# Performance work log

Measured on AMD Instinct MI355X. Metric: run time of the kernel, lower is better.

Reference implementation:

```python
import jax, jax.numpy as jnp
import numpy as np

H, D, K = 8, 64, 9           # new num heads, head size, conv kernel size
A = H * D                    # all_head_size = 512
HID = 2 * A                  # input hidden size = 1024
STD = 0.02


def setup_inputs() -> dict:
    key = jax.random.key(0)
    ks = jax.random.split(key, 16)
    B, S = 4, 2048
    f = jnp.float32
    inp = {
        'hidden_states': jax.random.normal(ks[0], (B, S, HID), f),
        'Wq': jax.random.normal(ks[1], (A, A), f) * STD,
        'bq': jnp.zeros((A,), f),
        'Wk': jax.random.normal(ks[2], (A, A), f) * STD,
        'bk': jnp.zeros((A,), f),
        'Wv': jax.random.normal(ks[3], (A, A), f) * STD,
        'bv': jnp.zeros((A,), f),
        'dw_w': jax.random.normal(ks[4], (A, 1, K), f) * STD,   # depthwise conv (groups=A)
        'pw_w': jax.random.normal(ks[5], (A, A, 1), f) * STD,   # pointwise 1x1 conv
        'sep_b': jnp.zeros((A, 1), f),                          # SeparableConv1D bias
        'Wck': jax.random.normal(ks[6], (H * K, A), f) * STD,   # conv_kernel_layer
        'bck': jnp.zeros((H * K,), f),
        'Wco': jax.random.normal(ks[7], (A, A), f) * STD,       # conv_out_layer
        'bco': jnp.zeros((A,), f),
    }
    return inp


def reference(hidden_states, Wq, bq, Wk, bk, Wv, bv, dw_w, pw_w, sep_b, Wck, bck, Wco, bco):
    B, S, _ = hidden_states.shape
    hs_attn = hidden_states[:, :, :A]
    hs_conv = hidden_states[:, :, A:]

    q = hs_attn @ Wq.T + bq
    k = hs_attn @ Wk.T + bk
    v = hs_attn @ Wv.T + bv

    # SeparableConv1D on (B, A, S): depthwise then pointwise, plus bias
    x = hs_conv.transpose(0, 2, 1)
    x = jax.lax.conv_general_dilated(
        x, dw_w, window_strides=(1,), padding=[(K // 2, K // 2)],
        feature_group_count=A, dimension_numbers=('NCH', 'OIH', 'NCH'))
    x = jnp.einsum('bcs,oc->bos', x, pw_w[:, :, 0]) + sep_b
    mixed_key_conv = x.transpose(0, 2, 1)            # (B,S,A)

    # per-token softmax conv kernel
    conv_attn = mixed_key_conv * hs_conv
    ckl = (conv_attn @ Wck.T + bck).reshape(B, S, H, K)
    ckl = jax.nn.softmax(ckl, axis=-1)               # softmax over kernel taps

    # dynamic-span lightweight convolution (unfold -> batched matmul)
    col = hs_conv @ Wco.T + bco                      # (B,S,A)
    pad = jnp.pad(col, ((0, 0), (K // 2, K // 2), (0, 0)))
    windows = jnp.stack([pad[:, i:i + S] for i in range(K)], axis=-1)  # (B,S,A,K)
    windows = windows.reshape(B, S, H, D, K)
    conv_out = jnp.einsum('bshdk,bshk->bshd', windows, ckl)            # (B,S,H,D)

    # standard self-attention
    qh = q.reshape(B, S, H, D).transpose(0, 2, 1, 3)
    kh = k.reshape(B, S, H, D).transpose(0, 2, 1, 3)
    vh = v.reshape(B, S, H, D).transpose(0, 2, 1, 3)
    scale = jnp.asarray(1.0 / np.sqrt(D), q.dtype)
    scores = jnp.einsum('bhqd,bhkd->bhqk', qh, kh) * scale
    probs = jax.nn.softmax(scores, axis=-1)
    ctx = jnp.einsum('bhqk,bhkd->bqhd', probs, vh)   # (B,S,H,D)

    out = jnp.concatenate([ctx, conv_out], axis=2)   # (B,S,2H,D)
    return out.reshape(B, S, HID)
```

## Files before the change

kernel.cpp:

```cpp
#include <hip/hip_runtime.h>
#include <hip/hip_bf16.h>

#define NH   8
#define HD   64
#define KW   9
#define AD   512
#define HIDD 1024
#define BB   4
#define SS   2048
#define MTOK (BB*SS)
#define WSZ  262144

typedef __attribute__((ext_vector_type(8))) short short8;
typedef __attribute__((ext_vector_type(4))) float floatx4;
typedef __attribute__((ext_vector_type(16))) float floatx16;

__device__ __forceinline__ short f2bf(float f) {
    unsigned u = __float_as_uint(f);
    u = (u + 0x7FFFu + ((u >> 16) & 1u)) >> 16;
    return (short)u;
}
__device__ __forceinline__ float bf2f(short s) {
    return __uint_as_float(((unsigned)(unsigned short)s) << 16);
}
__device__ __forceinline__ float exp2_raw(float x) {
    return __builtin_amdgcn_exp2f(x);
}
__device__ __forceinline__ unsigned pkbf2(float a, float b) {
    unsigned d;
    asm("v_cvt_pk_bf16_f32 %0, %1, %2" : "=v"(d) : "v"(a), "v"(b));
    return d;
}
__device__ __forceinline__ void gl2lds16(const short* g, short* l) {
    __builtin_amdgcn_global_load_lds(
        (const __attribute__((address_space(1))) void*)g,
        (__attribute__((address_space(3))) void*)l, 16, 0, 0);
}

__global__ __launch_bounds__(256) void prep_kernel(
    const float* __restrict__ hs,
    const float* __restrict__ pw, const float* __restrict__ Wco,
    const float* __restrict__ Wq, const float* __restrict__ Wk,
    const float* __restrict__ Wv, const float* __restrict__ Wck,
    const float* __restrict__ dw,
    short* __restrict__ hsb, short* __restrict__ wb, short* __restrict__ x1)
{
    __shared__ float wl[KW * AD];
    const int bid = blockIdx.x, tid = threadIdx.x;

    if (bid < 4096) {
        int idx = bid * 256 + tid;
        const float* s = hs + (long)idx * 8;
        float4 a = *(const float4*)s, c = *(const float4*)(s + 4);
        short8 o;
        o[0]=f2bf(a.x); o[1]=f2bf(a.y); o[2]=f2bf(a.z); o[3]=f2bf(a.w);
        o[4]=f2bf(c.x); o[5]=f2bf(c.y); o[6]=f2bf(c.z); o[7]=f2bf(c.w);
        *(short8*)(hsb + (long)idx * 8) = o;
    } else if (bid < 4768) {
        int idx = (bid - 4096) * 256 + tid;
        int e0 = idx * 8;
        short8 o;
        if (e0 < 5 * WSZ) {
            int w = e0 >> 18, off = e0 & (WSZ - 1);
            const float* src = (w == 0) ? pw : (w == 1) ? Wco : (w == 2) ? Wq
                             : (w == 3) ? Wk : Wv;
            float4 a = *(const float4*)(src + off), c = *(const float4*)(src + off + 4);
            o[0]=f2bf(a.x); o[1]=f2bf(a.y); o[2]=f2bf(a.z); o[3]=f2bf(a.w);
            o[4]=f2bf(c.x); o[5]=f2bf(c.y); o[6]=f2bf(c.z); o[7]=f2bf(c.w);
        } else {
            int off = e0 - 5 * WSZ;
            int row = off >> 9, col = off & 511;
            if (row < NH * KW) {
                const float* src = Wck + row * AD + col;
                float4 a = *(const float4*)src, c = *(const float4*)(src + 4);
                o[0]=f2bf(a.x); o[1]=f2bf(a.y); o[2]=f2bf(a.z); o[3]=f2bf(a.w);
                o[4]=f2bf(c.x); o[5]=f2bf(c.y); o[6]=f2bf(c.z); o[7]=f2bf(c.w);
            } else {
                for (int i = 0; i < 8; ++i) o[i] = 0;
            }
        }
        *(short8*)(wb + e0) = o;
    } else {
        for (int t = tid; t < KW * AD; t += 256) {
            int c = t / KW, k = t - c * KW;
            wl[k * AD + c] = dw[t];
        }
        __syncthreads();
        int idx = (bid - 4768) * 256 + tid;
        int c8  = (idx & 63) * 8;
        int tok = idx >> 6;
        int s   = tok & (SS - 1);
        int b   = tok >> 11;
        const float* base = hs + (long)(b * SS) * HIDD + AD + c8;
        float acc[8];
#pragma unroll
        for (int i = 0; i < 8; ++i) acc[i] = 0.f;
#pragma unroll
        for (int kk = 0; kk < KW; ++kk) {
            int ss2 = s + kk - KW / 2;
            if (ss2 >= 0 && ss2 < SS) {
                const float* hp = base + (long)ss2 * HIDD;
                float4 h0 = *(const float4*)hp;
                float4 h1 = *(const float4*)(hp + 4);
                float4 w0 = *(const float4*)(wl + kk * AD + c8);
                float4 w1 = *(const float4*)(wl + kk * AD + c8 + 4);
                acc[0] += w0.x * h0.x; acc[1] += w0.y * h0.y;
                acc[2] += w0.z * h0.z; acc[3] += w0.w * h0.w;
                acc[4] += w1.x * h1.x; acc[5] += w1.y * h1.y;
                acc[6] += w1.z * h1.z; acc[7] += w1.w * h1.w;
            }
        }
        short8 o;
#pragma unroll
        for (int i = 0; i < 8; ++i) o[i] = f2bf(acc[i]);
        *(short8*)(x1 + (long)tok * AD + c8) = o;
    }
}

template<int FM, int FN, int MODE>
__device__ __forceinline__ void gemm_body(
    int bx, int by, short* As, short* Bs,
    const short* __restrict__ X, int ldx, int xoff,
    const short* __restrict__ W,
    const float* __restrict__ b0p, const float* __restrict__ b1p,
    const float* __restrict__ b2p,
    const short* __restrict__ mulp, int mul_ld, int mul_off,
    void* __restrict__ Cout, short* __restrict__ vtout,
    int ldc, int N, int Kd, float oscale)
{
    constexpr int TM = 32 * FM, TN = 32 * FN;
    const int tid  = threadIdx.x;
    const int wv   = tid >> 6, lane = tid & 63;
    const int ln   = lane & 15, quad = lane >> 4;
    const int wm   = wv >> 1, wn = wv & 1;
    const int m0 = bx * TM, n0 = by * TN;

    floatx4 acc[FM][FN];
#pragma unroll
    for (int i = 0; i < FM; ++i)
#pragma unroll
        for (int j = 0; j < FN; ++j) acc[i][j] = (floatx4){0.f, 0.f, 0.f, 0.f};

    const short* xbase = X + (long)m0 * ldx + xoff;
    const short* wbase = W + (long)n0 * Kd;

    for (int k0 = 0; k0 < Kd; k0 += 64) {
#pragma unroll
        for (int g = tid; g < TM * 8; g += 256) {
            int m = g >> 3, p = g & 7, gk = p ^ (m & 7);
            gl2lds16(xbase + (long)m * ldx + k0 + gk * 8, &As[g * 8]);
        }
#pragma unroll
        for (int g = tid; g < TN * 8; g += 256) {
            int m = g >> 3, p = g & 7, gk = p ^ (m & 7);
            gl2lds16(wbase + (long)m * Kd + k0 + gk * 8, &Bs[g * 8]);
        }
        __syncthreads();
#pragma unroll
        for (int half = 0; half < 2; ++half) {
            short8 afr[FM], bfr[FN];
#pragma unroll
            for (int i = 0; i < FM; ++i) {
                int p = (half * 4 + quad) ^ (ln & 7);
                afr[i] = *(const short8*)&As[(wm * 16 * FM + i * 16 + ln) * 64 + p * 8];
            }
#pragma unroll
            for (int j = 0; j < FN; ++j) {
                int p = (half * 4 + quad) ^ (ln & 7);
                bfr[j] = *(const short8*)&Bs[(wn * 16 * FN + j * 16 + ln) * 64 + p * 8];
            }
#pragma unroll
            for (int i = 0; i < FM; ++i)
#pragma unroll
                for (int j = 0; j < FN; ++j)
                    acc[i][j] = __builtin_amdgcn_mfma_f32_16x16x32_bf16(
                        afr[i], bfr[j], acc[i][j], 0, 0, 0);
        }
        __syncthreads();
    }

#pragma unroll
    for (int j = 0; j < FN; ++j) {
        int n = n0 + wn * 16 * FN + j * 16 + ln;
        if constexpr (MODE == 3) {
            if (n >= 1024) {
                int hh = (n - 1024) >> 6, dd = (n - 1024) & 63;
                float bv = b2p[n - 1024];
                int mblk = m0 + wm * 16 * FM;
                int bidx = mblk >> 11, sblk = mblk & (SS - 1);
                short* dst = vtout + ((long)((bidx * NH + hh) * HD + dd)) * SS + sblk;
#pragma unroll
                for (int i = 0; i < FM; ++i) {
                    unsigned lo = pkbf2(acc[i][j][0] + bv, acc[i][j][1] + bv);
                    unsigned hi = pkbf2(acc[i][j][2] + bv, acc[i][j][3] + bv);
                    *(uint2*)(dst + i * 16 + quad * 4) = make_uint2(lo, hi);
                }
            } else {
                float bv = (n < 512) ? b0p[n] : b1p[n - 512];
                float sc = (n < 512) ? oscale : 1.f;
#pragma unroll
                for (int i = 0; i < FM; ++i) {
#pragma unroll
                    for (int r = 0; r < 4; ++r) {
                        int m = m0 + wm * 16 * FM + i * 16 + quad * 4 + r;
                        float val = (acc[i][j][r] + bv) * sc;
                        ((short*)Cout)[(long)m * ldc + n] = f2bf(val);
                    }
                }
            }
        } else if (n < N) {
            float bv = b0p[n], sc = oscale;
#pragma unroll
            for (int i = 0; i < FM; ++i) {
#pragma unroll
                for (int r = 0; r < 4; ++r) {
                    int m = m0 + wm * 16 * FM + i * 16 + quad * 4 + r;
                    float val = (acc[i][j][r] + bv) * sc;
                    if constexpr (MODE == 2)
                        val *= bf2f(mulp[(long)m * mul_ld + mul_off + n]);
                    if constexpr (MODE == 0)
                        ((float*)Cout)[(long)m * ldc + n] = val;
                    else
                        ((short*)Cout)[(long)m * ldc + n] = f2bf(val);
                }
            }
        }
    }
}

__global__ __launch_bounds__(256) void mega1_kernel(
    const short* __restrict__ hsb, const short* __restrict__ x1c,
    const short* __restrict__ Wqkv_b, const short* __restrict__ pw_b,
    const float* __restrict__ bq, const float* __restrict__ bk,
    const float* __restrict__ bv, const float* __restrict__ sepb,
    short* __restrict__ qkvb, short* __restrict__ vTb,
    short* __restrict__ cabO, float oscale)
{
    __shared__ __align__(16) short As[128 * 64];
    __shared__ __align__(16) short Bs[128 * 64];
    int bid = blockIdx.x;
    if (bid < 768) {
        gemm_body<4, 4, 3>(bid & 63, bid >> 6, As, Bs,
            hsb, HIDD, 0, Wqkv_b, bq, bk, bv, nullptr, 0, 0,
            qkvb, vTb, 1536, 1536, AD, oscale);
    } else {
        int id = bid - 768;
        gemm_body<4, 2, 2>(id & 63, id >> 6, As, Bs,
            x1c, AD, 0, pw_b, sepb, nullptr, nullptr, hsb, HIDD, AD,
            cabO, nullptr, AD, AD, AD, 1.f);
    }
}

__global__ __launch_bounds__(256) void mega2_kernel(
    const short* __restrict__ hsb, const short* __restrict__ cabO,
    const short* __restrict__ Wco_b, const short* __restrict__ Wck_b,
    const float* __restrict__ bco, const float* __restrict__ bck,
    short* __restrict__ x1c, float* __restrict__ ckl)
{
    __shared__ __align__(16) short As[128 * 64];
    __shared__ __align__(16) short Bs[128 * 64];
    int bid = blockIdx.x;
    if (bid < 512) {
        gemm_body<4, 2, 1>(bid & 63, bid >> 6, As, Bs,
            hsb, HIDD, AD, Wco_b, bco, nullptr, nullptr, nullptr, 0, 0,
            x1c, nullptr, AD, AD, AD, 1.f);
    } else {
        int id = bid - 512;
        gemm_body<2, 2, 0>(id & 127, id >> 7, As, Bs,
            cabO, AD, 0, Wck_b, bck, nullptr, nullptr, nullptr, 0, 0,
            ckl, nullptr, NH * KW, NH * KW, AD, 1.f);
    }
}

__global__ __launch_bounds__(256) void convout_kernel(
    const short* __restrict__ col, const float* __restrict__ ckl,
    float* __restrict__ out)
{
    int idx = blockIdx.x * 256 + threadIdx.x;
    int d4  = (idx & 127) * 4;
    int tok = idx >> 7;
    int s   = tok & (SS - 1);
    int b   = tok >> 11;
    int h   = d4 >> 6;
    const float* lg = ckl + (long)tok * (NH * KW) + h * KW;
    float wv[KW];
    float mx = -1e30f;
#pragma unroll
    for (int i = 0; i < KW; ++i) { wv[i] = lg[i]; mx = fmaxf(mx, wv[i]); }
    float sum = 0.f;
#pragma unroll
    for (int i = 0; i < KW; ++i) { wv[i] = __expf(wv[i] - mx); sum += wv[i]; }
    float inv = 1.f / sum;
    float a0 = 0.f, a1 = 0.f, a2 = 0.f, a3 = 0.f;
    const short* cbase = col + (long)(b * SS) * AD + d4;
#pragma unroll
    for (int kk = 0; kk < KW; ++kk) {
        int ss2 = s + kk - KW / 2;
        if (ss2 >= 0 && ss2 < SS) {
            uint2 cv = *(const uint2*)(cbase + (long)ss2 * AD);
            float w = wv[kk];
            a0 += w * bf2f((short)(cv.x & 0xFFFF));
            a1 += w * bf2f((short)(cv.x >> 16));
            a2 += w * bf2f((short)(cv.y & 0xFFFF));
            a3 += w * bf2f((short)(cv.y >> 16));
        }
    }
    *(float4*)&out[(long)tok * HIDD + AD + d4] =
        make_float4(a0 * inv, a1 * inv, a2 * inv, a3 * inv);
}

__global__ __launch_bounds__(256) void flash_mfma_kernel(
    const short* __restrict__ qkv, const short* __restrict__ vT,
    float* __restrict__ out)
{
    const int qt = blockIdx.x, h = blockIdx.y, b = blockIdx.z;
    const int tid  = threadIdx.x;
    const int w    = tid >> 6;
    const int lane = tid & 63;
    const int l5   = lane & 31;
    const int hh   = lane >> 5;

    __shared__ __align__(16) short Kb[3][4096];
    __shared__ __align__(16) short Vb[3][4096];
    __shared__ float ls[4][32];

    const int  q0 = qt * 128 + w * 32;
    const long rowbase = (long)b * SS;

    short8 qf[4];
    {
        const short* qrow = qkv + (rowbase + q0 + l5) * 1536 + h * HD;
#pragma unroll
        for (int i = 0; i < 4; ++i)
            qf[i] = *(const short8*)(qrow + i * 16 + hh * 8);
    }

    floatx16 acc0, acc1;
    floatx16 Z;
#pragma unroll
    for (int r = 0; r < 16; ++r) { acc0[r] = 0.f; acc1[r] = 0.f; Z[r] = 0.f; }
    float l_i = 0.f;

    const int m1 = tid >> 3,  gk1 = (tid & 7) ^ (m1 & 7);
    const int g2 = 256 + tid;
    const int m2 = g2 >> 3,   gk2 = (g2 & 7) ^ (m2 & 7);
    const short* kbase  = qkv + 512 + rowbase * 1536 + h * HD;
    const short* vtbase = vT + ((long)(b * NH + h) * HD) * SS;
    const short* sk0 = kbase  + (long)m1 * 1536 + gk1 * 8;
    const short* sk1 = kbase  + (long)m2 * 1536 + gk2 * 8;
    const short* sv0 = vtbase + (long)m1 * SS   + gk1 * 8;
    const short* sv1 = vtbase + (long)m2 * SS   + gk2 * 8;

    auto STAGE_K = [&](int slot, bool adv) {
        gl2lds16(sk0, &Kb[slot][tid * 8]);
        gl2lds16(sk1, &Kb[slot][g2 * 8]);
        if (adv) { sk0 += 64 * 1536; sk1 += 64 * 1536; }
    };
    auto STAGE_V = [&](int slot) {
        gl2lds16(sv0, &Vb[slot][tid * 8]);
        gl2lds16(sv1, &Vb[slot][g2 * 8]);
        sv0 += 64; sv1 += 64;
    };

    auto qkt = [&](const short* KB, floatx16& S0, floatx16& S1) {
        {
            int p = hh ^ (l5 & 7);
            short8 k0 = *(const short8*)&KB[l5 * 64 + p * 8];
            short8 k1 = *(const short8*)&KB[(32 + l5) * 64 + p * 8];
            S0 = __builtin_amdgcn_mfma_f32_32x32x16_bf16(k0, qf[0], Z, 0, 0, 0);
            S1 = __builtin_amdgcn_mfma_f32_32x32x16_bf16(k1, qf[0], Z, 0, 0, 0);
        }
#pragma unroll
        for (int i = 1; i < 4; ++i) {
            int p = (2 * i + hh) ^ (l5 & 7);
            short8 k0 = *(const short8*)&KB[l5 * 64 + p * 8];
            short8 k1 = *(const short8*)&KB[(32 + l5) * 64 + p * 8];
            S0 = __builtin_amdgcn_mfma_f32_32x32x16_bf16(k0, qf[i], S0, 0, 0, 0);
            S1 = __builtin_amdgcn_mfma_f32_32x32x16_bf16(k1, qf[i], S1, 0, 0, 0);
        }
    };

    auto smax = [&](const floatx16& S0, const floatx16& S1, short8* pf) {
        float pe0[16], pe1[16];
#pragma unroll
        for (int r = 0; r < 16; ++r) {
            pe0[r] = exp2_raw(S0[r]);
            pe1[r] = exp2_raw(S1[r]);
        }
        float s = 0.f;
#pragma unroll
        for (int r = 0; r < 16; ++r) s += pe0[r] + pe1[r];
        l_i += s;
#pragma unroll
        for (int t = 0; t < 2; ++t) {
            const float* pe = t ? pe1 : pe0;
#pragma unroll
            for (int u = 0; u < 2; ++u) {
                unsigned a0 = pkbf2(pe[8 * u + 0], pe[8 * u + 1]);
                unsigned a1 = pkbf2(pe[8 * u + 2], pe[8 * u + 3]);
                unsigned b0 = pkbf2(pe[8 * u + 4], pe[8 * u + 5]);
                unsigned b1 = pkbf2(pe[8 * u + 6], pe[8 * u + 7]);
                asm("v_permlane32_swap_b32 %0, %1" : "+v"(a0), "+v"(b0));
                asm("v_permlane32_swap_b32 %0, %1" : "+v"(a1), "+v"(b1));
                union { uint4 u4; short8 s8; } cv;
                cv.u4 = make_uint4(a0, a1, b0, b1);
                pf[t * 2 + u] = cv.s8;
            }
        }
    };

    auto pv = [&](const short* VB, const short8* pf) {
#pragma unroll
        for (int s = 0; s < 4; ++s) {
            int p = (2 * s + hh) ^ (l5 & 7);
            short8 v0 = *(const short8*)&VB[l5 * 64 + p * 8];
            short8 v1 = *(const short8*)&VB[(32 + l5) * 64 + p * 8];
            acc0 = __builtin_amdgcn_mfma_f32_32x32x16_bf16(pf[s], v0, acc0, 0, 0, 0);
            acc1 = __builtin_amdgcn_mfma_f32_32x32x16_bf16(pf[s], v1, acc1, 0, 0, 0);
        }
    };

    short8 pfA[4], pfB[4];

    STAGE_K(0, true);
    STAGE_K(1, true);
    STAGE_V(0);
    asm volatile("s_waitcnt vmcnt(0)" ::: "memory");
    __builtin_amdgcn_s_barrier();
    asm volatile("" ::: "memory");

    {
        STAGE_K(2, true);
        STAGE_V(1);
        floatx16 S0, S1;
        qkt(Kb[0], S0, S1);
        smax(S0, S1, pfA);
        asm volatile("s_waitcnt vmcnt(4)" ::: "memory");
        __builtin_amdgcn_s_barrier();
        asm volatile("" ::: "memory");
    }

#define PHASE(KS, VPS, KST, VST, KADV, PIN, POUT)                      \
    {                                                                  \
        STAGE_K(KST, KADV);                                            \
        STAGE_V(VST);                                                  \
        floatx16 S0, S1;                                               \
        __builtin_amdgcn_s_setprio(1);                                 \
        qkt(Kb[KS], S0, S1);                                           \
        pv(Vb[VPS], PIN);                                              \
        __builtin_amdgcn_s_setprio(0);                                 \
        smax(S0, S1, POUT);                                            \
        asm volatile("s_waitcnt vmcnt(4)" ::: "memory");               \
        __builtin_amdgcn_s_barrier();                                  \
        asm volatile("" ::: "memory");                                 \
    }

    for (int g = 0; g < 5; ++g) {
        bool notlast = (g < 4);
        PHASE(1, 0, 0, 2, true,    pfA, pfB);
        PHASE(2, 1, 1, 0, true,    pfB, pfA);
        PHASE(0, 2, 2, 1, true,    pfA, pfB);
        PHASE(1, 0, 0, 2, true,    pfB, pfA);
        PHASE(2, 1, 1, 0, notlast, pfA, pfB);
        PHASE(0, 2, 2, 1, notlast, pfB, pfA);
    }
#undef PHASE

    {
        floatx16 S0, S1;
        __builtin_amdgcn_s_setprio(1);
        qkt(Kb[1], S0, S1);
        pv(Vb[0], pfA);
        __builtin_amdgcn_s_setprio(0);
        smax(S0, S1, pfB);
        asm volatile("s_waitcnt vmcnt(0)" ::: "memory");
        __builtin_amdgcn_s_barrier();
        asm volatile("" ::: "memory");
    }
    pv(Vb[1], pfB);

    l_i += __shfl_xor(l_i, 32);
    ls[w][l5] = 1.f / l_i;
    float4 lv[4];
#pragma unroll
    for (int g = 0; g < 4; ++g)
        lv[g] = *(const float4*)&ls[w][8 * g + 4 * hh];

#pragma unroll
    for (int r = 0; r < 16; ++r) {
        int g = r >> 2, j = r & 3;
        int qr = j + 8 * g + 4 * hh;
        float iv = lv[g][j];
        float* orow = out + (rowbase + q0 + qr) * HIDD + h * HD;
        orow[l5]      = acc0[r] * iv;
        orow[32 + l5] = acc1[r] * iv;
    }
}

extern "C" void kernel_launch(void* const* d_in, const int* in_sizes, int n_in,
                              void* d_out, int out_size, void* d_ws, size_t ws_size,
                              hipStream_t stream)
{
    const float* hs   = (const float*)d_in[0];
    const float* Wq   = (const float*)d_in[1];
    const float* bq   = (const float*)d_in[2];
    const float* Wk   = (const float*)d_in[3];
    const float* bk   = (const float*)d_in[4];
    const float* Wv   = (const float*)d_in[5];
    const float* bv   = (const float*)d_in[6];
    const float* dw   = (const float*)d_in[7];
    const float* pw   = (const float*)d_in[8];
    const float* sepb = (const float*)d_in[9];
    const float* Wck  = (const float*)d_in[10];
    const float* bck  = (const float*)d_in[11];
    const float* Wco  = (const float*)d_in[12];
    const float* bco  = (const float*)d_in[13];
    float* out = (float*)d_out;

    short* hsb  = (short*)d_ws;
    short* x1c  = hsb + (long)MTOK * HIDD;
    short* qkvb = x1c + (long)MTOK * AD;
    short* vTb  = qkvb + (long)MTOK * 1536;
    float* ckl  = (float*)(vTb + (long)MTOK * AD);
    short* wb   = (short*)(ckl + (long)MTOK * (NH * KW));
    short* pw_b   = wb;
    short* Wco_b  = wb + 1L * WSZ;
    short* Wqkv_b = wb + 2L * WSZ;
    short* Wck_b  = wb + 5L * WSZ;
    short* cabO   = (short*)d_out;

    const float QSCALE = 0.18033688011112042f;

    prep_kernel<<<6816, 256, 0, stream>>>(
        hs, pw, Wco, Wq, Wk, Wv, Wck, dw, hsb, wb, x1c);
    mega1_kernel<<<1280, 256, 0, stream>>>(
        hsb, x1c, Wqkv_b, pw_b, bq, bk, bv, sepb, qkvb, vTb, cabO, QSCALE);
    mega2_kernel<<<768, 256, 0, stream>>>(
        hsb, cabO, Wco_b, Wck_b, bco, bck, x1c, ckl);
    convout_kernel<<<MTOK * AD / 1024, 256, 0, stream>>>(x1c, ckl, out);
    flash_mfma_kernel<<<dim3(SS / 128, NH, BB), 256, 0, stream>>>(qkvb, vTb, out);

    (void)in_sizes; (void)n_in; (void)out_size; (void)ws_size;
}
```

Measured before the change: 212.6 us.

## Fuse conv-out and flash attention into one 512-thread tail kernel

Merges the lightweight-conv output kernel and the flash attention kernel into a single launch. The first 256 blocks run attention and the remaining 2048 blocks run the conv-out. Each attention block now has 8 waves covering 256 queries, and each thread stages one K and one V chunk per tile instead of two, so the waitcnt thresholds drop to match. This removes a launch and lets the memory-bound conv work overlap with the MFMA-bound attention. In exchange there are fewer, larger attention blocks, which may cut occupancy and load balance.

```diff
diff --git a/kernel.cpp b/kernel.cpp
--- a/kernel.cpp
+++ b/kernel.cpp
@@ -272,59 +272,60 @@
     }
 }
 
-__global__ __launch_bounds__(256) void convout_kernel(
-    const short* __restrict__ col, const float* __restrict__ ckl,
+__global__ __launch_bounds__(512) void tail_kernel(
+    const short* __restrict__ qkv, const short* __restrict__ vT,
+    const short* __restrict__ colb, const float* __restrict__ cklp,
     float* __restrict__ out)
 {
-    int idx = blockIdx.x * 256 + threadIdx.x;
-    int d4  = (idx & 127) * 4;
-    int tok = idx >> 7;
-    int s   = tok & (SS - 1);
-    int b   = tok >> 11;
-    int h   = d4 >> 6;
-    const float* lg = ckl + (long)tok * (NH * KW) + h * KW;
-    float wv[KW];
-    float mx = -1e30f;
-#pragma unroll
-    for (int i = 0; i < KW; ++i) { wv[i] = lg[i]; mx = fmaxf(mx, wv[i]); }
-    float sum = 0.f;
-#pragma unroll
-    for (int i = 0; i < KW; ++i) { wv[i] = __expf(wv[i] - mx); sum += wv[i]; }
-    float inv = 1.f / sum;
-    float a0 = 0.f, a1 = 0.f, a2 = 0.f, a3 = 0.f;
-    const short* cbase = col + (long)(b * SS) * AD + d4;
-#pragma unroll
-    for (int kk = 0; kk < KW; ++kk) {
-        int ss2 = s + kk - KW / 2;
-        if (ss2 >= 0 && ss2 < SS) {
-            uint2 cv = *(const uint2*)(cbase + (long)ss2 * AD);
-            float w = wv[kk];
-            a0 += w * bf2f((short)(cv.x & 0xFFFF));
-            a1 += w * bf2f((short)(cv.x >> 16));
-            a2 += w * bf2f((short)(cv.y & 0xFFFF));
-            a3 += w * bf2f((short)(cv.y >> 16));
-        }
-    }
-    *(float4*)&out[(long)tok * HIDD + AD + d4] =
-        make_float4(a0 * inv, a1 * inv, a2 * inv, a3 * inv);
-}
-
-__global__ __launch_bounds__(256) void flash_mfma_kernel(
-    const short* __restrict__ qkv, const short* __restrict__ vT,
-    float* __restrict__ out)
-{
-    const int qt = blockIdx.x, h = blockIdx.y, b = blockIdx.z;
-    const int tid  = threadIdx.x;
+    __shared__ __align__(16) short Kb[3][4096];
+    __shared__ __align__(16) short Vb[3][4096];
+    __shared__ float ls[8][32];
+
+    const int bid = blockIdx.x;
+    const int tid = threadIdx.x;
+
+    if (bid >= 256) {
+        int idx = (bid - 256) * 512 + tid;
+        int d4  = (idx & 127) * 4;
+        int tok = idx >> 7;
+        int s   = tok & (SS - 1);
+        int b   = tok >> 11;
+        int h   = d4 >> 6;
+        const float* lg = cklp + (long)tok * (NH * KW) + h * KW;
+        float wv[KW];
+        float mx = -1e30f;
+#pragma unroll
+        for (int i = 0; i < KW; ++i) { wv[i] = lg[i]; mx = fmaxf(mx, wv[i]); }
+        float sum = 0.f;
+#pragma unroll
+        for (int i = 0; i < KW; ++i) { wv[i] = __expf(wv[i] - mx); sum += wv[i]; }
+        float inv = 1.f / sum;
+        float a0 = 0.f, a1 = 0.f, a2 = 0.f, a3 = 0.f;
+        const short* cbase = colb + (long)(b * SS) * AD + d4;
+#pragma unroll
+        for (int kk = 0; kk < KW; ++kk) {
+            int ss2 = s + kk - KW / 2;
+            if (ss2 >= 0 && ss2 < SS) {
+                uint2 cv = *(const uint2*)(cbase + (long)ss2 * AD);
+                float w = wv[kk];
+                a0 += w * bf2f((short)(cv.x & 0xFFFF));
+                a1 += w * bf2f((short)(cv.x >> 16));
+                a2 += w * bf2f((short)(cv.y & 0xFFFF));
+                a3 += w * bf2f((short)(cv.y >> 16));
+            }
+        }
+        *(float4*)&out[(long)tok * HIDD + AD + d4] =
+            make_float4(a0 * inv, a1 * inv, a2 * inv, a3 * inv);
+        return;
+    }
+
+    const int qt = bid & 7, h = (bid >> 3) & 7, b = bid >> 6;
     const int w    = tid >> 6;
     const int lane = tid & 63;
     const int l5   = lane & 31;
     const int hh   = lane >> 5;
 
-    __shared__ __align__(16) short Kb[3][4096];
-    __shared__ __align__(16) short Vb[3][4096];
-    __shared__ float ls[4][32];
-
-    const int  q0 = qt * 128 + w * 32;
+    const int  q0 = qt * 256 + w * 32;
     const long rowbase = (long)b * SS;
 
     short8 qf[4];
@@ -341,25 +342,19 @@
     for (int r = 0; r < 16; ++r) { acc0[r] = 0.f; acc1[r] = 0.f; Z[r] = 0.f; }
     float l_i = 0.f;
 
-    const int m1 = tid >> 3,  gk1 = (tid & 7) ^ (m1 & 7);
-    const int g2 = 256 + tid;
-    const int m2 = g2 >> 3,   gk2 = (g2 & 7) ^ (m2 & 7);
+    const int m1 = tid >> 3, gk1 = (tid & 7) ^ (m1 & 7);
     const short* kbase  = qkv + 512 + rowbase * 1536 + h * HD;
     const short* vtbase = vT + ((long)(b * NH + h) * HD) * SS;
     const short* sk0 = kbase  + (long)m1 * 1536 + gk1 * 8;
-    const short* sk1 = kbase  + (long)m2 * 1536 + gk2 * 8;
     const short* sv0 = vtbase + (long)m1 * SS   + gk1 * 8;
-    const short* sv1 = vtbase + (long)m2 * SS   + gk2 * 8;
 
     auto STAGE_K = [&](int slot, bool adv) {
         gl2lds16(sk0, &Kb[slot][tid * 8]);
-        gl2lds16(sk1, &Kb[slot][g2 * 8]);
-        if (adv) { sk0 += 64 * 1536; sk1 += 64 * 1536; }
+        if (adv) sk0 += 64 * 1536;
     };
     auto STAGE_V = [&](int slot) {
         gl2lds16(sv0, &Vb[slot][tid * 8]);
-        gl2lds16(sv1, &Vb[slot][g2 * 8]);
-        sv0 += 64; sv1 += 64;
+        sv0 += 64;
     };
 
     auto qkt = [&](const short* KB, floatx16& S0, floatx16& S1) {
@@ -435,7 +430,7 @@
         floatx16 S0, S1;
         qkt(Kb[0], S0, S1);
         smax(S0, S1, pfA);
-        asm volatile("s_waitcnt vmcnt(4)" ::: "memory");
+        asm volatile("s_waitcnt vmcnt(2)" ::: "memory");
         __builtin_amdgcn_s_barrier();
         asm volatile("" ::: "memory");
     }
@@ -450,7 +445,7 @@
         pv(Vb[VPS], PIN);                                              \
         __builtin_amdgcn_s_setprio(0);                                 \
         smax(S0, S1, POUT);                                            \
-        asm volatile("s_waitcnt vmcnt(4)" ::: "memory");               \
+        asm volatile("s_waitcnt vmcnt(2)" ::: "memory");               \
         __builtin_amdgcn_s_barrier();                                  \
         asm volatile("" ::: "memory");                                 \
     }
@@ -537,8 +532,7 @@
         hsb, x1c, Wqkv_b, pw_b, bq, bk, bv, sepb, qkvb, vTb, cabO, QSCALE);
     mega2_kernel<<<768, 256, 0, stream>>>(
         hsb, cabO, Wco_b, Wck_b, bco, bck, x1c, ckl);
-    convout_kernel<<<MTOK * AD / 1024, 256, 0, stream>>>(x1c, ckl, out);
-    flash_mfma_kernel<<<dim3(SS / 128, NH, BB), 256, 0, stream>>>(qkvb, vTb, out);
+    tail_kernel<<<2304, 512, 0, stream>>>(qkvb, vTb, x1c, ckl, out);
 
     (void)in_sizes; (void)n_in; (void)out_size; (void)ws_size;
 }
```

Result: slower. 223.2 us (+5.0%).

## Co-schedule flash attention with Wco/Wck GEMMs in one launch

Applied to the files above, without the earlier changes.

Merges the flash-attention kernel and the Wco and Wck projection GEMMs into a single kernel, mega3. Blocks 0–511 run attention and the rest run the GEMMs, so the GEMM work can fill the tail of the attention kernel and one launch is removed. The intermediate cabO buffer is moved into the conv half of the output rows (row stride 2048 shorts), so concurrent attention writes to the attn half cannot clobber it. The pointwise GEMM in mega1 switches to 4x4 tiles, which halves its block count. The risks are load imbalance from the mixed block types and a larger shared-memory footprint per block.

```diff
diff --git a/kernel.cpp b/kernel.cpp
--- a/kernel.cpp
+++ b/kernel.cpp
@@ -245,30 +245,221 @@
             qkvb, vTb, 1536, 1536, AD, oscale);
     } else {
         int id = bid - 768;
-        gemm_body<4, 2, 2>(id & 63, id >> 6, As, Bs,
+        gemm_body<4, 4, 2>(id & 63, id >> 6, As, Bs,
             x1c, AD, 0, pw_b, sepb, nullptr, nullptr, hsb, HIDD, AD,
-            cabO, nullptr, AD, AD, AD, 1.f);
-    }
-}
-
-__global__ __launch_bounds__(256) void mega2_kernel(
+            cabO, nullptr, 2048, AD, AD, 1.f);
+    }
+}
+
+__global__ __launch_bounds__(256) void mega3_kernel(
+    const short* __restrict__ qkv, const short* __restrict__ vT,
     const short* __restrict__ hsb, const short* __restrict__ cabO,
     const short* __restrict__ Wco_b, const short* __restrict__ Wck_b,
     const float* __restrict__ bco, const float* __restrict__ bck,
-    short* __restrict__ x1c, float* __restrict__ ckl)
+    short* __restrict__ x1c, float* __restrict__ cklp,
+    float* __restrict__ out)
 {
-    __shared__ __align__(16) short As[128 * 64];
-    __shared__ __align__(16) short Bs[128 * 64];
-    int bid = blockIdx.x;
-    if (bid < 512) {
-        gemm_body<4, 2, 1>(bid & 63, bid >> 6, As, Bs,
-            hsb, HIDD, AD, Wco_b, bco, nullptr, nullptr, nullptr, 0, 0,
-            x1c, nullptr, AD, AD, AD, 1.f);
-    } else {
-        int id = bid - 512;
-        gemm_body<2, 2, 0>(id & 127, id >> 7, As, Bs,
-            cabO, AD, 0, Wck_b, bck, nullptr, nullptr, nullptr, 0, 0,
-            ckl, nullptr, NH * KW, NH * KW, AD, 1.f);
+    __shared__ __align__(16) char smem[49664];
+    const int bid = blockIdx.x;
+    const int tid = threadIdx.x;
+
+    if (bid >= 512) {
+        short* As = (short*)smem;
+        short* Bs = (short*)smem + 128 * 64;
+        if (bid < 768) {
+            int id = bid - 512;
+            gemm_body<4, 4, 1>(id & 63, id >> 6, As, Bs,
+                hsb, HIDD, AD, Wco_b, bco, nullptr, nullptr, nullptr, 0, 0,
+                x1c, nullptr, AD, AD, AD, 1.f);
+        } else {
+            int id = bid - 768;
+            gemm_body<2, 2, 0>(id & 127, id >> 7, As, Bs,
+                cabO, 2048, 0, Wck_b, bck, nullptr, nullptr, nullptr, 0, 0,
+                cklp, nullptr, NH * KW, NH * KW, AD, 1.f);
+        }
+        return;
+    }
+
+    short* const KbB = (short*)smem;
+    short* const VbB = (short*)smem + 3 * 4096;
+    float* const ls  = (float*)(smem + 49152);
+
+    const int qt = bid & 15, h = (bid >> 4) & 7, b = bid >> 7;
+    const int w    = tid >> 6;
+    const int lane = tid & 63;
+    const int l5   = lane & 31;
+    const int hh   = lane >> 5;
+
+    const int  q0 = qt * 128 + w * 32;
+    const long rowbase = (long)b * SS;
+
+    short8 qf[4];
+    {
+        const short* qrow = qkv + (rowbase + q0 + l5) * 1536 + h * HD;
+#pragma unroll
+        for (int i = 0; i < 4; ++i)
+            qf[i] = *(const short8*)(qrow + i * 16 + hh * 8);
+    }
+
+    floatx16 acc0, acc1;
+    floatx16 Z;
+#pragma unroll
+    for (int r = 0; r < 16; ++r) { acc0[r] = 0.f; acc1[r] = 0.f; Z[r] = 0.f; }
+    float l_i = 0.f;
+
+    const int m1 = tid >> 3,  gk1 = (tid & 7) ^ (m1 & 7);
+    const int g2 = 256 + tid;
+    const int m2 = g2 >> 3,   gk2 = (g2 & 7) ^ (m2 & 7);
+    const short* kbase  = qkv + 512 + rowbase * 1536 + h * HD;
+    const short* vtbase = vT + ((long)(b * NH + h) * HD) * SS;
+    const short* sk0 = kbase  + (long)m1 * 1536 + gk1 * 8;
+    const short* sk1 = kbase  + (long)m2 * 1536 + gk2 * 8;
+    const short* sv0 = vtbase + (long)m1 * SS   + gk1 * 8;
+    const short* sv1 = vtbase + (long)m2 * SS   + gk2 * 8;
+
+    auto STAGE_K = [&](int slot, bool adv) {
+        gl2lds16(sk0, KbB + slot * 4096 + tid * 8);
+        gl2lds16(sk1, KbB + slot * 4096 + g2 * 8);
+        if (adv) { sk0 += 64 * 1536; sk1 += 64 * 1536; }
+    };
+    auto STAGE_V = [&](int slot) {
+        gl2lds16(sv0, VbB + slot * 4096 + tid * 8);
+        gl2lds16(sv1, VbB + slot * 4096 + g2 * 8);
+        sv0 += 64; sv1 += 64;
+    };
+
+    auto qkt = [&](const short* KB, floatx16& S0, floatx16& S1) {
+        {
+            int p = hh ^ (l5 & 7);
+            short8 k0 = *(const short8*)&KB[l5 * 64 + p * 8];
+            short8 k1 = *(const short8*)&KB[(32 + l5) * 64 + p * 8];
+            S0 = __builtin_amdgcn_mfma_f32_32x32x16_bf16(k0, qf[0], Z, 0, 0, 0);
+            S1 = __builtin_amdgcn_mfma_f32_32x32x16_bf16(k1, qf[0], Z, 0, 0, 0);
+        }
+#pragma unroll
+        for (int i = 1; i < 4; ++i) {
+            int p = (2 * i + hh) ^ (l5 & 7);
+            short8 k0 = *(const short8*)&KB[l5 * 64 + p * 8];
+            short8 k1 = *(const short8*)&KB[(32 + l5) * 64 + p * 8];
+            S0 = __builtin_amdgcn_mfma_f32_32x32x16_bf16(k0, qf[i], S0, 0, 0, 0);
+            S1 = __builtin_amdgcn_mfma_f32_32x32x16_bf16(k1, qf[i], S1, 0, 0, 0);
+        }
+    };
+
+    auto smax = [&](const floatx16& S0, const floatx16& S1, short8* pf) {
+        float pe0[16], pe1[16];
+#pragma unroll
+        for (int r = 0; r < 16; ++r) {
+            pe0[r] = exp2_raw(S0[r]);
+            pe1[r] = exp2_raw(S1[r]);
+        }
+        float s = 0.f;
+#pragma unroll
+        for (int r = 0; r < 16; ++r) s += pe0[r] + pe1[r];
+        l_i += s;
+#pragma unroll
+        for (int t = 0; t < 2; ++t) {
+            const float* pe = t ? pe1 : pe0;
+#pragma unroll
+            for (int u = 0; u < 2; ++u) {
+                unsigned a0 = pkbf2(pe[8 * u + 0], pe[8 * u + 1]);
+                unsigned a1 = pkbf2(pe[8 * u + 2], pe[8 * u + 3]);
+                unsigned b0 = pkbf2(pe[8 * u + 4], pe[8 * u + 5]);
+                unsigned b1 = pkbf2(pe[8 * u + 6], pe[8 * u + 7]);
+                asm("v_permlane32_swap_b32 %0, %1" : "+v"(a0), "+v"(b0));
+                asm("v_permlane32_swap_b32 %0, %1" : "+v"(a1), "+v"(b1));
+                union { uint4 u4; short8 s8; } cv;
+                cv.u4 = make_uint4(a0, a1, b0, b1);
+                pf[t * 2 + u] = cv.s8;
+            }
+        }
+    };
+
+    auto pv = [&](const short* VB, const short8* pf) {
+#pragma unroll
+        for (int s = 0; s < 4; ++s) {
+            int p = (2 * s + hh) ^ (l5 & 7);
+            short8 v0 = *(const short8*)&VB[l5 * 64 + p * 8];
+            short8 v1 = *(const short8*)&VB[(32 + l5) * 64 + p * 8];
+            acc0 = __builtin_amdgcn_mfma_f32_32x32x16_bf16(pf[s], v0, acc0, 0, 0, 0);
+            acc1 = __builtin_amdgcn_mfma_f32_32x32x16_bf16(pf[s], v1, acc1, 0, 0, 0);
+        }
+    };
+
+    short8 pfA[4], pfB[4];
+
+    STAGE_K(0, true);
+    STAGE_K(1, true);
+    STAGE_V(0);
+    asm volatile("s_waitcnt vmcnt(0)" ::: "memory");
+    __builtin_amdgcn_s_barrier();
+    asm volatile("" ::: "memory");
+
+    {
+        STAGE_K(2, true);
+        STAGE_V(1);
+        floatx16 S0, S1;
+        qkt(KbB, S0, S1);
+        smax(S0, S1, pfA);
+        asm volatile("s_waitcnt vmcnt(4)" ::: "memory");
+        __builtin_amdgcn_s_barrier();
+        asm volatile("" ::: "memory");
+    }
+
+#define PHASE(KS, VPS, KST, VST, KADV, PIN, POUT)                      \
+    {                                                                  \
+        STAGE_K(KST, KADV);                                            \
+        STAGE_V(VST);                                                  \
+        floatx16 S0, S1;                                               \
+        __builtin_amdgcn_s_setprio(1);                                 \
+        qkt(KbB + (KS) * 4096, S0, S1);                                \
+        pv(VbB + (VPS) * 4096, PIN);                                   \
+        __builtin_amdgcn_s_setprio(0);                                 \
+        smax(S0, S1, POUT);                                            \
+        asm volatile("s_waitcnt vmcnt(4)" ::: "memory");               \
+        __builtin_amdgcn_s_barrier();                                  \
+        asm volatile("" ::: "memory");                                 \
+    }
+
+    for (int g = 0; g < 5; ++g) {
+        bool notlast = (g < 4);
+        PHASE(1, 0, 0, 2, true,    pfA, pfB);
+        PHASE(2, 1, 1, 0, true,    pfB, pfA);
+        PHASE(0, 2, 2, 1, true,    pfA, pfB);
+        PHASE(1, 0, 0, 2, true,    pfB, pfA);
+        PHASE(2, 1, 1, 0, notlast, pfA, pfB);
+        PHASE(0, 2, 2, 1, notlast, pfB, pfA);
+    }
+#undef PHASE
+
+    {
+        floatx16 S0, S1;
+        __builtin_amdgcn_s_setprio(1);
+        qkt(KbB + 1 * 4096, S0, S1);
+        pv(VbB + 0 * 4096, pfA);
+        __builtin_amdgcn_s_setprio(0);
+        smax(S0, S1, pfB);
+        asm volatile("s_waitcnt vmcnt(0)" ::: "memory");
+        __builtin_amdgcn_s_barrier();
+        asm volatile("" ::: "memory");
+    }
+    pv(VbB + 1 * 4096, pfB);
+
+    l_i += __shfl_xor(l_i, 32);
+    ls[w * 32 + l5] = 1.f / l_i;
+    float4 lv[4];
+#pragma unroll
+    for (int g = 0; g < 4; ++g)
+        lv[g] = *(const float4*)&ls[w * 32 + 8 * g + 4 * hh];
+
+#pragma unroll
+    for (int r = 0; r < 16; ++r) {
+        int g = r >> 2, j = r & 3;
+        int qr = j + 8 * g + 4 * hh;
+        float iv = lv[g][j];
+        float* orow = out + (rowbase + q0 + qr) * HIDD + h * HD;
+        orow[l5]      = acc0[r] * iv;
+        orow[32 + l5] = acc1[r] * iv;
     }
 }
 
@@ -307,194 +498,6 @@
     }
     *(float4*)&out[(long)tok * HIDD + AD + d4] =
         make_float4(a0 * inv, a1 * inv, a2 * inv, a3 * inv);
-}
-
-__global__ __launch_bounds__(256) void flash_mfma_kernel(
-    const short* __restrict__ qkv, const short* __restrict__ vT,
-    float* __restrict__ out)
-{
-    const int qt = blockIdx.x, h = blockIdx.y, b = blockIdx.z;
-    const int tid  = threadIdx.x;
-    const int w    = tid >> 6;
-    const int lane = tid & 63;
-    const int l5   = lane & 31;
-    const int hh   = lane >> 5;
-
-    __shared__ __align__(16) short Kb[3][4096];
-    __shared__ __align__(16) short Vb[3][4096];
-    __shared__ float ls[4][32];
-
-    const int  q0 = qt * 128 + w * 32;
-    const long rowbase = (long)b * SS;
-
-    short8 qf[4];
-    {
-        const short* qrow = qkv + (rowbase + q0 + l5) * 1536 + h * HD;
-#pragma unroll
-        for (int i = 0; i < 4; ++i)
-            qf[i] = *(const short8*)(qrow + i * 16 + hh * 8);
-    }
-
-    floatx16 acc0, acc1;
-    floatx16 Z;
-#pragma unroll
-    for (int r = 0; r < 16; ++r) { acc0[r] = 0.f; acc1[r] = 0.f; Z[r] = 0.f; }
-    float l_i = 0.f;
-
-    const int m1 = tid >> 3,  gk1 = (tid & 7) ^ (m1 & 7);
-    const int g2 = 256 + tid;
-    const int m2 = g2 >> 3,   gk2 = (g2 & 7) ^ (m2 & 7);
-    const short* kbase  = qkv + 512 + rowbase * 1536 + h * HD;
-    const short* vtbase = vT + ((long)(b * NH + h) * HD) * SS;
-    const short* sk0 = kbase  + (long)m1 * 1536 + gk1 * 8;
-    const short* sk1 = kbase  + (long)m2 * 1536 + gk2 * 8;
-    const short* sv0 = vtbase + (long)m1 * SS   + gk1 * 8;
-    const short* sv1 = vtbase + (long)m2 * SS   + gk2 * 8;
-
-    auto STAGE_K = [&](int slot, bool adv) {
-        gl2lds16(sk0, &Kb[slot][tid * 8]);
-        gl2lds16(sk1, &Kb[slot][g2 * 8]);
-        if (adv) { sk0 += 64 * 1536; sk1 += 64 * 1536; }
-    };
-    auto STAGE_V = [&](int slot) {
-        gl2lds16(sv0, &Vb[slot][tid * 8]);
-        gl2lds16(sv1, &Vb[slot][g2 * 8]);
-        sv0 += 64; sv1 += 64;
-    };
-
-    auto qkt = [&](const short* KB, floatx16& S0, floatx16& S1) {
-        {
-            int p = hh ^ (l5 & 7);
-            short8 k0 = *(const short8*)&KB[l5 * 64 + p * 8];
-            short8 k1 = *(const short8*)&KB[(32 + l5) * 64 + p * 8];
-            S0 = __builtin_amdgcn_mfma_f32_32x32x16_bf16(k0, qf[0], Z, 0, 0, 0);
-            S1 = __builtin_amdgcn_mfma_f32_32x32x16_bf16(k1, qf[0], Z, 0, 0, 0);
-        }
-#pragma unroll
-        for (int i = 1; i < 4; ++i) {
-            int p = (2 * i + hh) ^ (l5 & 7);
-            short8 k0 = *(const short8*)&KB[l5 * 64 + p * 8];
-            short8 k1 = *(const short8*)&KB[(32 + l5) * 64 + p * 8];
-            S0 = __builtin_amdgcn_mfma_f32_32x32x16_bf16(k0, qf[i], S0, 0, 0, 0);
-            S1 = __builtin_amdgcn_mfma_f32_32x32x16_bf16(k1, qf[i], S1, 0, 0, 0);
-        }
-    };
-
-    auto smax = [&](const floatx16& S0, const floatx16& S1, short8* pf) {
-        float pe0[16], pe1[16];
-#pragma unroll
-        for (int r = 0; r < 16; ++r) {
-            pe0[r] = exp2_raw(S0[r]);
-            pe1[r] = exp2_raw(S1[r]);
-        }
-        float s = 0.f;
-#pragma unroll
-        for (int r = 0; r < 16; ++r) s += pe0[r] + pe1[r];
-        l_i += s;
-#pragma unroll
-        for (int t = 0; t < 2; ++t) {
-            const float* pe = t ? pe1 : pe0;
-#pragma unroll
-            for (int u = 0; u < 2; ++u) {
-                unsigned a0 = pkbf2(pe[8 * u + 0], pe[8 * u + 1]);
-                unsigned a1 = pkbf2(pe[8 * u + 2], pe[8 * u + 3]);
-                unsigned b0 = pkbf2(pe[8 * u + 4], pe[8 * u + 5]);
-                unsigned b1 = pkbf2(pe[8 * u + 6], pe[8 * u + 7]);
-                asm("v_permlane32_swap_b32 %0, %1" : "+v"(a0), "+v"(b0));
-                asm("v_permlane32_swap_b32 %0, %1" : "+v"(a1), "+v"(b1));
-                union { uint4 u4; short8 s8; } cv;
-                cv.u4 = make_uint4(a0, a1, b0, b1);
-                pf[t * 2 + u] = cv.s8;
-            }
-        }
-    };
-
-    auto pv = [&](const short* VB, const short8* pf) {
-#pragma unroll
-        for (int s = 0; s < 4; ++s) {
-            int p = (2 * s + hh) ^ (l5 & 7);
-            short8 v0 = *(const short8*)&VB[l5 * 64 + p * 8];
-            short8 v1 = *(const short8*)&VB[(32 + l5) * 64 + p * 8];
-            acc0 = __builtin_amdgcn_mfma_f32_32x32x16_bf16(pf[s], v0, acc0, 0, 0, 0);
-            acc1 = __builtin_amdgcn_mfma_f32_32x32x16_bf16(pf[s], v1, acc1, 0, 0, 0);
-        }
-    };
-
-    short8 pfA[4], pfB[4];
-
-    STAGE_K(0, true);
-    STAGE_K(1, true);
-    STAGE_V(0);
-    asm volatile("s_waitcnt vmcnt(0)" ::: "memory");
-    __builtin_amdgcn_s_barrier();
-    asm volatile("" ::: "memory");
-
-    {
-        STAGE_K(2, true);
-        STAGE_V(1);
-        floatx16 S0, S1;
-        qkt(Kb[0], S0, S1);
-        smax(S0, S1, pfA);
-        asm volatile("s_waitcnt vmcnt(4)" ::: "memory");
-        __builtin_amdgcn_s_barrier();
-        asm volatile("" ::: "memory");
-    }
-
-#define PHASE(KS, VPS, KST, VST, KADV, PIN, POUT)                      \
-    {                                                                  \
-        STAGE_K(KST, KADV);                                            \
-        STAGE_V(VST);                                                  \
-        floatx16 S0, S1;                                               \
-        __builtin_amdgcn_s_setprio(1);                                 \
-        qkt(Kb[KS], S0, S1);                                           \
-        pv(Vb[VPS], PIN);                                              \
-        __builtin_amdgcn_s_setprio(0);                                 \
-        smax(S0, S1, POUT);                                            \
-        asm volatile("s_waitcnt vmcnt(4)" ::: "memory");               \
-        __builtin_amdgcn_s_barrier();                                  \
-        asm volatile("" ::: "memory");                                 \
-    }
-
-    for (int g = 0; g < 5; ++g) {
-        bool notlast = (g < 4);
-        PHASE(1, 0, 0, 2, true,    pfA, pfB);
-        PHASE(2, 1, 1, 0, true,    pfB, pfA);
-        PHASE(0, 2, 2, 1, true,    pfA, pfB);
-        PHASE(1, 0, 0, 2, true,    pfB, pfA);
-        PHASE(2, 1, 1, 0, notlast, pfA, pfB);
-        PHASE(0, 2, 2, 1, notlast, pfB, pfA);
-    }
-#undef PHASE
-
-    {
-        floatx16 S0, S1;
-        __builtin_amdgcn_s_setprio(1);
-        qkt(Kb[1], S0, S1);
-        pv(Vb[0], pfA);
-        __builtin_amdgcn_s_setprio(0);
-        smax(S0, S1, pfB);
-        asm volatile("s_waitcnt vmcnt(0)" ::: "memory");
-        __builtin_amdgcn_s_barrier();
-        asm volatile("" ::: "memory");
-    }
-    pv(Vb[1], pfB);
-
-    l_i += __shfl_xor(l_i, 32);
-    ls[w][l5] = 1.f / l_i;
-    float4 lv[4];
-#pragma unroll
-    for (int g = 0; g < 4; ++g)
-        lv[g] = *(const float4*)&ls[w][8 * g + 4 * hh];
-
-#pragma unroll
-    for (int r = 0; r < 16; ++r) {
-        int g = r >> 2, j = r & 3;
-        int qr = j + 8 * g + 4 * hh;
-        float iv = lv[g][j];
-        float* orow = out + (rowbase + q0 + qr) * HIDD + h * HD;
-        orow[l5]      = acc0[r] * iv;
-        orow[32 + l5] = acc1[r] * iv;
-    }
 }
 
 extern "C" void kernel_launch(void* const* d_in, const int* in_sizes, int n_in,
@@ -527,18 +530,17 @@
     short* Wco_b  = wb + 1L * WSZ;
     short* Wqkv_b = wb + 2L * WSZ;
     short* Wck_b  = wb + 5L * WSZ;
-    short* cabO   = (short*)d_out;
+    short* cabO   = (short*)d_out + 1024;
 
     const float QSCALE = 0.18033688011112042f;
 
     prep_kernel<<<6816, 256, 0, stream>>>(
         hs, pw, Wco, Wq, Wk, Wv, Wck, dw, hsb, wb, x1c);
-    mega1_kernel<<<1280, 256, 0, stream>>>(
+    mega1_kernel<<<1024, 256, 0, stream>>>(
         hsb, x1c, Wqkv_b, pw_b, bq, bk, bv, sepb, qkvb, vTb, cabO, QSCALE);
-    mega2_kernel<<<768, 256, 0, stream>>>(
-        hsb, cabO, Wco_b, Wck_b, bco, bck, x1c, ckl);
+    mega3_kernel<<<1024, 256, 0, stream>>>(
+        qkvb, vTb, hsb, cabO, Wco_b, Wck_b, bco, bck, x1c, ckl, out);
     convout_kernel<<<MTOK * AD / 1024, 256, 0, stream>>>(x1c, ckl, out);
-    flash_mfma_kernel<<<dim3(SS / 128, NH, BB), 256, 0, stream>>>(qkvb, vTb, out);
 
     (void)in_sizes; (void)n_in; (void)out_size; (void)ws_size;
 }
```

After: 211.6 us. About the same (-0.5%).
